# Kernel tuning notes

Hardware: AMD Instinct MI355X
Metric: run time of the kernel (lower is better)

Reference implementation:

```python
import jax, jax.numpy as jnp
import numpy as np

N_NODES = 50000
N_EDGES = 800000
HIDDEN = 128
N_GRAPHS = 32
EPS = 1e-5  # GraphNorm eps


def setup_inputs() -> dict:
    key = jax.random.key(0)
    ks = jax.random.split(key, 8)
    x = jax.random.normal(ks[0], (N_NODES, HIDDEN), dtype=jnp.float32)
    edge_index = jax.random.randint(ks[1], (2, N_EDGES), 0, N_NODES, dtype=jnp.int64)
    batch = jnp.sort(jax.random.randint(ks[2], (N_NODES,), 0, N_GRAPHS, dtype=jnp.int64))
    s = 1.0 / np.sqrt(HIDDEN)
    # SAGEConv: lin_l (applied to aggregated neighbors, with bias) and lin_r (root, no bias)
    W_l = jax.random.normal(ks[3], (HIDDEN, HIDDEN), dtype=jnp.float32) * s
    b_l = jnp.zeros((HIDDEN,), dtype=jnp.float32)
    W_r = jax.random.normal(ks[4], (HIDDEN, HIDDEN), dtype=jnp.float32) * s
    # GraphNorm params: weight, bias, mean_scale (alpha)
    gn_weight = jnp.ones((HIDDEN,), dtype=jnp.float32)
    gn_bias = jnp.zeros((HIDDEN,), dtype=jnp.float32)
    gn_mean_scale = jnp.ones((HIDDEN,), dtype=jnp.float32)
    return {
        "x": x, "edge_index": edge_index, "batch": batch,
        "W_l": W_l, "b_l": b_l, "W_r": W_r,
        "gn_weight": gn_weight, "gn_bias": gn_bias, "gn_mean_scale": gn_mean_scale,
    }


def reference(x, edge_index, batch, W_l, b_l, W_r, gn_weight, gn_bias, gn_mean_scale):
    src, dst = edge_index[0], edge_index[1]
    n = x.shape[0]
    # --- SAGEConv: mean aggregation of source features at destination ---
    msg_sum = jax.ops.segment_sum(x[src], dst, num_segments=n)          # [N, D]
    deg = jax.ops.segment_sum(jnp.ones((src.shape[0],), x.dtype), dst, num_segments=n)
    agg = msg_sum / jnp.maximum(deg, 1.0)[:, None]
    out = agg @ W_l + b_l + x @ W_r                                      # [N, D]
    # --- GraphNorm: per-graph mean/var with learnable mean scale alpha ---
    g_cnt = jax.ops.segment_sum(jnp.ones((n,), x.dtype), batch, num_segments=N_GRAPHS)[:, None]
    g_cnt = jnp.maximum(g_cnt, 1.0)
    mean = jax.ops.segment_sum(out, batch, num_segments=N_GRAPHS) / g_cnt  # [G, D]
    sub = out - gn_mean_scale * mean[batch]
    var = jax.ops.segment_sum(sub * sub, batch, num_segments=N_GRAPHS) / g_cnt
    normed = gn_weight * sub / jnp.sqrt(var[batch] + EPS) + gn_bias
    # --- exact GELU (torch nn.GELU default), dropout = identity (eval), residual ---
    return jax.nn.gelu(normed, approximate=False) + x
```

## Files before the change

### kernel.cpp

```cpp
#include <hip/hip_runtime.h>
#include <math.h>

#define NN 50000
#define NE 800000
#define HD 128
#define NG 32
#define GN_EPS 1e-5f
#define NSH 8

#define NBLK_R 250
#define CH_R   3200
#define NBUCK  196
#define NBB    (NBUCK * NBLK_R)
#define NCHS   ((NBB + 255) / 256)
#define DCAP   8192
#define PREP_BLKS 3125

typedef __bf16 v8bf __attribute__((ext_vector_type(8)));
typedef float f32x4 __attribute__((ext_vector_type(4)));

#define ROWPTR_OFF 0
#define BB_OFF     50016
#define CS_OFF     99016
#define GSUMS_OFF  99280
#define GSQS_OFF   132048
#define GCNTS_OFF  164816
#define MEAN_OFF   165072
#define RSTD_OFF   169168
#define SRCS_OFF   173264
#define PSRC_OFF   573264
#define PDLOW_OFF  973264
#define WPACK_OFF  1173264
#define ABUF_OFF   1189648
#define OBF_OFF    7589648
#define MEMSET_INTS (32768 + 32768 + 256)

__device__ __forceinline__ unsigned short f2bf(float f) {
  unsigned int u = __float_as_uint(f);
  u = (u + 0x7fffu + ((u >> 16) & 1u)) >> 16;
  return (unsigned short)u;
}
__device__ __forceinline__ float bf_lo(unsigned int u) { return __uint_as_float(u << 16); }
__device__ __forceinline__ float bf_hi(unsigned int u) { return __uint_as_float(u & 0xffff0000u); }

__global__ __launch_bounds__(256) void prep_rhist_k(const float* __restrict__ x,
    const float* __restrict__ Wl, const float* __restrict__ Wr,
    unsigned short* __restrict__ Abuf, unsigned short* __restrict__ wp,
    int* __restrict__ zbase, const int* __restrict__ ei, int* __restrict__ bb) {
  __shared__ int h[NBUCK];
  int tid = threadIdx.x;
  if (blockIdx.x < PREP_BLKS) {
    int i = blockIdx.x * 256 + tid;
    if (i < MEMSET_INTS) zbase[i] = 0;
    if (i < 32768) {
      int e = i & 7, lane = (i >> 3) & 63, nt = (i >> 9) & 7, ks = i >> 12;
      int k = ks * 32 + (lane >> 4) * 8 + e;
      int c = nt * 16 + (lane & 15);
      float v = (k < HD) ? Wl[k * HD + c] : Wr[(k - HD) * HD + c];
      wp[i] = f2bf(v);
    }
    if (i < NN * 16) {
      int n = i >> 4, seg = i & 15;
      const float* src = x + (size_t)n * HD + seg * 8;
      float4 v0 = *(const float4*)(src);
      float4 v1 = *(const float4*)(src + 4);
      uint4 o;
      o.x = (unsigned)f2bf(v0.x) | ((unsigned)f2bf(v0.y) << 16);
      o.y = (unsigned)f2bf(v0.z) | ((unsigned)f2bf(v0.w) << 16);
      o.z = (unsigned)f2bf(v1.x) | ((unsigned)f2bf(v1.y) << 16);
      o.w = (unsigned)f2bf(v1.z) | ((unsigned)f2bf(v1.w) << 16);
      *(uint4*)(Abuf + (size_t)n * 256 + 128 + seg * 8) = o;
    }
  } else {
    int b = blockIdx.x - PREP_BLKS;
    for (int i = tid; i < NBUCK; i += 256) h[i] = 0;
    __syncthreads();
    int base = b * CH_R;
    for (int j = tid; j < CH_R / 4; j += 256) {
      int4 d = *(const int4*)(ei + NE + base + j * 4);
      atomicAdd(&h[d.x >> 8], 1);
      atomicAdd(&h[d.y >> 8], 1);
      atomicAdd(&h[d.z >> 8], 1);
      atomicAdd(&h[d.w >> 8], 1);
    }
    __syncthreads();
    for (int i = tid; i < NBUCK; i += 256) bb[i * NBLK_R + b] = h[i];
  }
}

__global__ __launch_bounds__(256) void csum_k(const int* __restrict__ bb,
                                              int* __restrict__ cs) {
  __shared__ int red[4];
  int i = blockIdx.x * 256 + threadIdx.x;
  int v = (i < NBB) ? bb[i] : 0;
#pragma unroll
  for (int off = 32; off; off >>= 1) v += __shfl_down(v, off, 64);
  if ((threadIdx.x & 63) == 0) red[threadIdx.x >> 6] = v;
  __syncthreads();
  if (threadIdx.x == 0) cs[blockIdx.x] = red[0] + red[1] + red[2] + red[3];
}

__global__ __launch_bounds__(256) void cfill_k(int* __restrict__ bb,
                                               const int* __restrict__ cs) {
  __shared__ int sb[256];
  __shared__ int s[256];
  int t = threadIdx.x;
  sb[t] = (t < NCHS) ? cs[t] : 0;
  int i = blockIdx.x * 256 + t;
  int c = (i < NBB) ? bb[i] : 0;
  s[t] = c;
  __syncthreads();
#pragma unroll
  for (int off = 1; off < 256; off <<= 1) {
    int u1 = (t >= off) ? sb[t - off] : 0;
    int u2 = (t >= off) ? s[t - off] : 0;
    __syncthreads();
    sb[t] += u1;
    s[t] += u2;
    __syncthreads();
  }
  int chunkpre = (blockIdx.x == 0) ? 0 : sb[blockIdx.x - 1];
  if (i < NBB) bb[i] = chunkpre + s[t] - c;
}

__global__ __launch_bounds__(256) void rscatter_k(const int* __restrict__ ei,
    const int* __restrict__ bb, unsigned short* __restrict__ psrc,
    unsigned char* __restrict__ pdlow) {
  __shared__ int cur[NBUCK];
  int tid = threadIdx.x, b = blockIdx.x;
  for (int i = tid; i < NBUCK; i += 256) cur[i] = bb[i * NBLK_R + b];
  __syncthreads();
  int base = b * CH_R;
  for (int j = tid; j < CH_R / 4; j += 256) {
    int4 s4 = *(const int4*)(ei + base + j * 4);
    int4 d4 = *(const int4*)(ei + NE + base + j * 4);
    int p;
    p = atomicAdd(&cur[d4.x >> 8], 1); psrc[p] = (unsigned short)s4.x; pdlow[p] = (unsigned char)(d4.x & 255);
    p = atomicAdd(&cur[d4.y >> 8], 1); psrc[p] = (unsigned short)s4.y; pdlow[p] = (unsigned char)(d4.y & 255);
    p = atomicAdd(&cur[d4.z >> 8], 1); psrc[p] = (unsigned short)s4.z; pdlow[p] = (unsigned char)(d4.z & 255);
    p = atomicAdd(&cur[d4.w >> 8], 1); psrc[p] = (unsigned short)s4.w; pdlow[p] = (unsigned char)(d4.w & 255);
  }
}

__global__ __launch_bounds__(256) void rfinal_k(const int* __restrict__ bb,
    const unsigned short* __restrict__ psrc, const unsigned char* __restrict__ pdlow,
    unsigned short* __restrict__ srcs, int* __restrict__ rowptr) {
  __shared__ unsigned short ssrc[DCAP];
  __shared__ unsigned short sout[DCAP];
  __shared__ unsigned char sdl[DCAP];
  __shared__ int h2[256], scn[256], cur2[256];
  int tid = threadIdx.x, k = blockIdx.x;
  int segB = bb[k * NBLK_R];
  int segE = (k == NBUCK - 1) ? NE : bb[(k + 1) * NBLK_R];
  int cnt = segE - segB;
  for (int j = tid; j < cnt; j += 256) {
    ssrc[j] = psrc[segB + j];
    sdl[j] = pdlow[segB + j];
  }
  h2[tid] = 0;
  __syncthreads();
  for (int j = tid; j < cnt; j += 256) atomicAdd(&h2[sdl[j]], 1);
  __syncthreads();
  scn[tid] = h2[tid];
  __syncthreads();
#pragma unroll
  for (int off = 1; off < 256; off <<= 1) {
    int u = (tid >= off) ? scn[tid - off] : 0;
    __syncthreads();
    scn[tid] += u;
    __syncthreads();
  }
  int excl = scn[tid] - h2[tid];
  cur2[tid] = excl;
  int dst = k * 256 + tid;
  if (dst < NN) rowptr[dst] = segB + excl;
  if (dst == NN - 1) rowptr[NN] = NE;
  __syncthreads();
  for (int j = tid; j < cnt; j += 256) {
    int p = atomicAdd(&cur2[sdl[j]], 1);
    sout[p] = ssrc[j];
  }
  __syncthreads();
  for (int j = tid; j < cnt; j += 256) srcs[segB + j] = sout[j];
}

__global__ __launch_bounds__(256) void gather_k(const int* __restrict__ rowptr,
    const unsigned short* __restrict__ srcs, unsigned short* Abuf) {
  int t = blockIdx.x * 256 + threadIdx.x;
  int n = t >> 4, q = t & 15;
  if (n >= NN) return;
  int b = rowptr[n], e = rowptr[n + 1];
  float a0=0,a1=0,a2=0,a3=0,a4=0,a5=0,a6=0,a7=0;
  int i = b;
  for (; i + 1 < e; i += 2) {
    int s0 = srcs[i], s1 = srcs[i + 1];
    uint4 v0 = *(const uint4*)(Abuf + (size_t)s0 * 256 + 128 + q * 8);
    uint4 v1 = *(const uint4*)(Abuf + (size_t)s1 * 256 + 128 + q * 8);
    a0 += bf_lo(v0.x) + bf_lo(v1.x);  a1 += bf_hi(v0.x) + bf_hi(v1.x);
    a2 += bf_lo(v0.y) + bf_lo(v1.y);  a3 += bf_hi(v0.y) + bf_hi(v1.y);
    a4 += bf_lo(v0.z) + bf_lo(v1.z);  a5 += bf_hi(v0.z) + bf_hi(v1.z);
    a6 += bf_lo(v0.w) + bf_lo(v1.w);  a7 += bf_hi(v0.w) + bf_hi(v1.w);
  }
  if (i < e) {
    int s0 = srcs[i];
    uint4 v0 = *(const uint4*)(Abuf + (size_t)s0 * 256 + 128 + q * 8);
    a0 += bf_lo(v0.x); a1 += bf_hi(v0.x);
    a2 += bf_lo(v0.y); a3 += bf_hi(v0.y);
    a4 += bf_lo(v0.z); a5 += bf_hi(v0.z);
    a6 += bf_lo(v0.w); a7 += bf_hi(v0.w);
  }
  float inv = 1.0f / fmaxf((float)(e - b), 1.0f);
  uint4 o;
  o.x = (unsigned)f2bf(a0 * inv) | ((unsigned)f2bf(a1 * inv) << 16);
  o.y = (unsigned)f2bf(a2 * inv) | ((unsigned)f2bf(a3 * inv) << 16);
  o.z = (unsigned)f2bf(a4 * inv) | ((unsigned)f2bf(a5 * inv) << 16);
  o.w = (unsigned)f2bf(a6 * inv) | ((unsigned)f2bf(a7 * inv) << 16);
  *(uint4*)(Abuf + (size_t)n * 256 + q * 8) = o;
}

__global__ __launch_bounds__(256) void gemm_k(const unsigned short* __restrict__ Abuf,
    const unsigned short* __restrict__ wp, const float* __restrict__ bl,
    const int* __restrict__ batch, unsigned short* __restrict__ obf,
    float* __restrict__ gsumS, float* __restrict__ gsqS,
    float* __restrict__ gcntS) {
  __shared__ float lsum[16][136];
  __shared__ float lsq[16][136];
  __shared__ unsigned char ridx[64];
  __shared__ int sg0, snrun;
  int tid = threadIdx.x;
  int base0 = blockIdx.x * 64;
  int nvalid = min(64, NN - base0);
  if (tid == 0) {
    int g0 = batch[base0];
    sg0 = g0;
    snrun = batch[base0 + nvalid - 1] - g0 + 1;
  }
  __syncthreads();
  if (tid < 64)
    ridx[tid] = (tid < nvalid) ? (unsigned char)(batch[base0 + tid] - sg0)
                               : (unsigned char)0;
  __syncthreads();

  int shard = blockIdx.x & 7;
  float* gs = gsumS + shard * (NG * HD);
  float* gq = gsqS + shard * (NG * HD);
  float* gc = gcntS + shard * NG;

  int wave = tid >> 6;
  int lane = tid & 63;
  int base = base0 + wave * 16;
  int row = lane & 15, kg = lane >> 4;
  int node = base + row;
  if (node > NN - 1) node = NN - 1;
  const unsigned short* arow = Abuf + (size_t)node * 256 + kg * 8;
  f32x4 acc[8] = {};
#pragma unroll
  for (int ks = 0; ks < 8; ++ks) {
    v8bf a = __builtin_bit_cast(v8bf, *(const uint4*)(arow + ks * 32));
    const unsigned short* wrow = wp + ks * 4096 + lane * 8;
#pragma unroll
    for (int nt = 0; nt < 8; ++nt) {
      v8bf b = __builtin_bit_cast(v8bf, *(const uint4*)(wrow + nt * 512));
      acc[nt] = __builtin_amdgcn_mfma_f32_16x16x32_bf16(a, b, acc[nt], 0, 0, 0);
    }
  }
  int c0 = lane & 15;
  float bv[8];
#pragma unroll
  for (int nt = 0; nt < 8; ++nt) bv[nt] = bl[nt * 16 + c0];

  if (snrun == 1) {
    float ps0[8] = {}, pq0[8] = {};
#pragma unroll
    for (int j = 0; j < 4; ++j) {
      int n = base0 + wave * 16 + kg * 4 + j;
      if (n >= NN) break;
      unsigned short* orow = obf + (size_t)n * HD;
#pragma unroll
      for (int nt = 0; nt < 8; ++nt) {
        float v = acc[nt][j] + bv[nt];
        orow[nt * 16 + c0] = f2bf(v);
        ps0[nt] += v;
        pq0[nt] += v * v;
      }
    }
    int r = wave * 4 + kg;
#pragma unroll
    for (int nt = 0; nt < 8; ++nt) {
      lsum[r][nt * 16 + c0] = ps0[nt];
      lsq[r][nt * 16 + c0] = pq0[nt];
    }
    __syncthreads();
    if (tid < HD) {
      float s = 0.0f, q = 0.0f;
#pragma unroll
      for (int r2 = 0; r2 < 16; ++r2) { s += lsum[r2][tid]; q += lsq[r2][tid]; }
      atomicAdd(gs + sg0 * HD + tid, s);
      atomicAdd(gq + sg0 * HD + tid, q);
    }
    if (tid == 0) atomicAdd(gc + sg0, (float)nvalid);
  } else if (snrun == 2) {
    float ps0[8] = {}, pq0[8] = {}, ps1[8] = {}, pq1[8] = {};
#pragma unroll
    for (int j = 0; j < 4; ++j) {
      int rb = wave * 16 + kg * 4 + j;
      int n = base0 + rb;
      if (n >= NN) break;
      unsigned short* orow = obf + (size_t)n * HD;
      bool b1 = (ridx[rb] != 0);
#pragma unroll
      for (int nt = 0; nt < 8; ++nt) {
        float v = acc[nt][j] + bv[nt];
        orow[nt * 16 + c0] = f2bf(v);
        if (b1) { ps1[nt] += v; pq1[nt] += v * v; }
        else    { ps0[nt] += v; pq0[nt] += v * v; }
      }
    }
    int r = wave * 4 + kg;
#pragma unroll
    for (int nt = 0; nt < 8; ++nt) {
      lsum[r][nt * 16 + c0] = ps0[nt];
      lsq[r][nt * 16 + c0] = pq0[nt];
    }
    __syncthreads();
    if (tid < HD) {
      float s = 0.0f, q = 0.0f;
#pragma unroll
      for (int r2 = 0; r2 < 16; ++r2) { s += lsum[r2][tid]; q += lsq[r2][tid]; }
      atomicAdd(gs + sg0 * HD + tid, s);
      atomicAdd(gq + sg0 * HD + tid, q);
    }
    __syncthreads();
#pragma unroll
    for (int nt = 0; nt < 8; ++nt) {
      lsum[r][nt * 16 + c0] = ps1[nt];
      lsq[r][nt * 16 + c0] = pq1[nt];
    }
    __syncthreads();
    if (tid < HD) {
      float s = 0.0f, q = 0.0f;
#pragma unroll
      for (int r2 = 0; r2 < 16; ++r2) { s += lsum[r2][tid]; q += lsq[r2][tid]; }
      atomicAdd(gs + (sg0 + 1) * HD + tid, s);
      atomicAdd(gq + (sg0 + 1) * HD + tid, q);
    }
    if (tid == 0) {
      int n0 = 0;
      for (int r2 = 0; r2 < nvalid; ++r2) n0 += (ridx[r2] == 0);
      atomicAdd(gc + sg0, (float)n0);
      atomicAdd(gc + sg0 + 1, (float)(nvalid - n0));
    }
  } else {
#pragma unroll
    for (int j = 0; j < 4; ++j) {
      int rb = wave * 16 + kg * 4 + j;
      int n = base0 + rb;
      if (n >= NN) break;
      unsigned short* orow = obf + (size_t)n * HD;
      int g = sg0 + ridx[rb];
#pragma unroll
      for (int nt = 0; nt < 8; ++nt) {
        float v = acc[nt][j] + bv[nt];
        orow[nt * 16 + c0] = f2bf(v);
        atomicAdd(gs + g * HD + nt * 16 + c0, v);
        atomicAdd(gq + g * HD + nt * 16 + c0, v * v);
      }
    }
    if (tid < nvalid) atomicAdd(gc + batch[base0 + tid], 1.0f);
  }
}

__global__ __launch_bounds__(256) void finalize_k(const float* __restrict__ gsumS,
    const float* __restrict__ gsqS, const float* __restrict__ gcntS,
    const float* __restrict__ alpha, float* __restrict__ mean,
    float* __restrict__ rstd) {
  int i = blockIdx.x * 256 + threadIdx.x;
  if (i >= NG * HD) return;
  int g = i >> 7, d = i & 127;
  float s = 0.0f, q = 0.0f, cnt = 0.0f;
#pragma unroll
  for (int sh = 0; sh < NSH; ++sh) {
    s += gsumS[sh * (NG * HD) + i];
    q += gsqS[sh * (NG * HD) + i];
    cnt += gcntS[sh * NG + g];
  }
  cnt = fmaxf(cnt, 1.0f);
  float mu = s / cnt;
  float a = alpha[d];
  float var = q / cnt - mu * mu * (2.0f * a - a * a);
  mean[i] = mu;
  rstd[i] = rsqrtf(fmaxf(var, 0.0f) + GN_EPS);
}

__global__ __launch_bounds__(256) void final_k(const unsigned short* __restrict__ obf,
    float* __restrict__ out, const float* __restrict__ x,
    const int* __restrict__ batch, const float* __restrict__ mean,
    const float* __restrict__ rstd, const float* __restrict__ alpha,
    const float* __restrict__ gw, const float* __restrict__ gb) {
  size_t i = ((size_t)blockIdx.x * 256 + threadIdx.x) * 4;
  if (i >= (size_t)NN * HD) return;
  int n = (int)(i >> 7);
  int d = (int)(i & 127);
  int g = batch[n];
  uint2 ov = *(const uint2*)(obf + i);
  float4 xv = *(const float4*)(x + i);
  float4 al = *(const float4*)(alpha + d);
  float4 w  = *(const float4*)(gw + d);
  float4 b  = *(const float4*)(gb + d);
  float4 mn = *(const float4*)(mean + (size_t)g * HD + d);
  float4 rs = *(const float4*)(rstd + (size_t)g * HD + d);
  float vv[4] = {bf_lo(ov.x), bf_hi(ov.x), bf_lo(ov.y), bf_hi(ov.y)};
  float xx[4] = {xv.x, xv.y, xv.z, xv.w};
  float aa[4] = {al.x, al.y, al.z, al.w};
  float ww[4] = {w.x, w.y, w.z, w.w};
  float bb2[4] = {b.x, b.y, b.z, b.w};
  float mm[4] = {mn.x, mn.y, mn.z, mn.w};
  float rr[4] = {rs.x, rs.y, rs.z, rs.w};
  float r[4];
#pragma unroll
  for (int c = 0; c < 4; ++c) {
    float sub = vv[c] - aa[c] * mm[c];
    float nm  = ww[c] * sub * rr[c] + bb2[c];
    float ge  = 0.5f * nm * (1.0f + erff(nm * 0.70710678118654752f));
    r[c] = ge + xx[c];
  }
  float4 res = {r[0], r[1], r[2], r[3]};
  *(float4*)(out + i) = res;
}

extern "C" void kernel_launch(void* const* d_in, const int* in_sizes, int n_in,
                              void* d_out, int out_size, void* d_ws, size_t ws_size,
                              hipStream_t stream) {
  const float* x     = (const float*)d_in[0];
  const int*   ei    = (const int*)d_in[1];
  const int*   batch = (const int*)d_in[2];
  const float* Wl    = (const float*)d_in[3];
  const float* bl    = (const float*)d_in[4];
  const float* Wr    = (const float*)d_in[5];
  const float* gw    = (const float*)d_in[6];
  const float* gb    = (const float*)d_in[7];
  const float* alpha = (const float*)d_in[8];

  float* out = (float*)d_out;
  int*   wsi = (int*)d_ws;
  float* wsf = (float*)d_ws;
  int* rowptr = wsi + ROWPTR_OFF;
  int* bb     = wsi + BB_OFF;
  int* cs     = wsi + CS_OFF;
  float* gsumS = wsf + GSUMS_OFF;
  float* gsqS  = wsf + GSQS_OFF;
  float* gcntS = wsf + GCNTS_OFF;
  float* mean  = wsf + MEAN_OFF;
  float* rstd  = wsf + RSTD_OFF;
  unsigned short* srcs  = (unsigned short*)(wsi + SRCS_OFF);
  unsigned short* psrc  = (unsigned short*)(wsi + PSRC_OFF);
  unsigned char*  pdlow = (unsigned char*)(wsi + PDLOW_OFF);
  unsigned short* wpack = (unsigned short*)(wsi + WPACK_OFF);
  unsigned short* Abuf  = (unsigned short*)(wsi + ABUF_OFF);
  unsigned short* obf   = (unsigned short*)(wsi + OBF_OFF);

  prep_rhist_k<<<PREP_BLKS + NBLK_R, 256, 0, stream>>>(
      x, Wl, Wr, Abuf, wpack, (int*)(wsf + GSUMS_OFF), ei, bb);

  csum_k<<<NCHS, 256, 0, stream>>>(bb, cs);
  cfill_k<<<NCHS, 256, 0, stream>>>(bb, cs);
  rscatter_k<<<NBLK_R, 256, 0, stream>>>(ei, bb, psrc, pdlow);
  rfinal_k<<<NBUCK, 256, 0, stream>>>(bb, psrc, pdlow, srcs, rowptr);

  gather_k<<<(NN * 16 + 255) / 256, 256, 0, stream>>>(rowptr, srcs, Abuf);

  gemm_k<<<(NN + 63) / 64, 256, 0, stream>>>(Abuf, wpack, bl, batch, obf,
                                             gsumS, gsqS, gcntS);

  finalize_k<<<16, 256, 0, stream>>>(gsumS, gsqS, gcntS, alpha, mean, rstd);

  final_k<<<(NN * HD / 4 + 255) / 256, 256, 0, stream>>>(
      obf, out, x, batch, mean, rstd, alpha, gw, gb);
}
```

Before: 108.4 us.

## Partition neighbor gather by source range and enlarge radix sort block count

The gather kernel now makes four passes over each node's edge list and in each pass loads only source rows from one quarter of the node range. The aim is to keep concurrently accessed rows within a cache-sized window. The radix histogram and scatter stages use 800 blocks of 1000 edges instead of 250 of 3200, and the scan kernel moves to 1024-thread blocks to cover the larger bucket-by-block table. In exchange, the edge index list is read four times per node with a branch per edge, and the prefix scan has more entries to process.

```diff
diff --git a/kernel.cpp b/kernel.cpp
--- a/kernel.cpp
+++ b/kernel.cpp
@@ -8,31 +8,34 @@
 #define GN_EPS 1e-5f
 #define NSH 8
 
-#define NBLK_R 250
-#define CH_R   3200
+#define NBLK_R 800
+#define CH_R   1000
 #define NBUCK  196
 #define NBB    (NBUCK * NBLK_R)
 #define NCHS   ((NBB + 255) / 256)
 #define DCAP   8192
 #define PREP_BLKS 3125
 
+#define GP 4
+#define GW (NN / GP)
+
 typedef __bf16 v8bf __attribute__((ext_vector_type(8)));
 typedef float f32x4 __attribute__((ext_vector_type(4)));
 
 #define ROWPTR_OFF 0
 #define BB_OFF     50016
-#define CS_OFF     99016
-#define GSUMS_OFF  99280
-#define GSQS_OFF   132048
-#define GCNTS_OFF  164816
-#define MEAN_OFF   165072
-#define RSTD_OFF   169168
-#define SRCS_OFF   173264
-#define PSRC_OFF   573264
-#define PDLOW_OFF  973264
-#define WPACK_OFF  1173264
-#define ABUF_OFF   1189648
-#define OBF_OFF    7589648
+#define CS_OFF     206816
+#define GSUMS_OFF  207840
+#define GSQS_OFF   240608
+#define GCNTS_OFF  273376
+#define MEAN_OFF   273632
+#define RSTD_OFF   277728
+#define SRCS_OFF   281824
+#define PSRC_OFF   681824
+#define PDLOW_OFF  1081824
+#define WPACK_OFF  1281824
+#define ABUF_OFF   1298208
+#define OBF_OFF    7698208
 #define MEMSET_INTS (32768 + 32768 + 256)
 
 __device__ __forceinline__ unsigned short f2bf(float f) {
@@ -76,8 +79,8 @@
     for (int i = tid; i < NBUCK; i += 256) h[i] = 0;
     __syncthreads();
     int base = b * CH_R;
-    for (int j = tid; j < CH_R / 4; j += 256) {
-      int4 d = *(const int4*)(ei + NE + base + j * 4);
+    if (tid < CH_R / 4) {
+      int4 d = *(const int4*)(ei + NE + base + tid * 4);
       atomicAdd(&h[d.x >> 8], 1);
       atomicAdd(&h[d.y >> 8], 1);
       atomicAdd(&h[d.z >> 8], 1);
@@ -100,18 +103,17 @@
   if (threadIdx.x == 0) cs[blockIdx.x] = red[0] + red[1] + red[2] + red[3];
 }
 
-__global__ __launch_bounds__(256) void cfill_k(int* __restrict__ bb,
-                                               const int* __restrict__ cs) {
-  __shared__ int sb[256];
-  __shared__ int s[256];
+__global__ __launch_bounds__(1024) void cfill_k(int* __restrict__ bb,
+                                                const int* __restrict__ cs) {
+  __shared__ int sb[1024];
+  __shared__ int s[1024];
   int t = threadIdx.x;
   sb[t] = (t < NCHS) ? cs[t] : 0;
-  int i = blockIdx.x * 256 + t;
+  int i = blockIdx.x * 1024 + t;
   int c = (i < NBB) ? bb[i] : 0;
   s[t] = c;
   __syncthreads();
-#pragma unroll
-  for (int off = 1; off < 256; off <<= 1) {
+  for (int off = 1; off < 1024; off <<= 1) {
     int u1 = (t >= off) ? sb[t - off] : 0;
     int u2 = (t >= off) ? s[t - off] : 0;
     __syncthreads();
@@ -119,7 +121,7 @@
     s[t] += u2;
     __syncthreads();
   }
-  int chunkpre = (blockIdx.x == 0) ? 0 : sb[blockIdx.x - 1];
+  int chunkpre = (blockIdx.x == 0) ? 0 : sb[blockIdx.x * 4 - 1];
   if (i < NBB) bb[i] = chunkpre + s[t] - c;
 }
 
@@ -131,9 +133,9 @@
   for (int i = tid; i < NBUCK; i += 256) cur[i] = bb[i * NBLK_R + b];
   __syncthreads();
   int base = b * CH_R;
-  for (int j = tid; j < CH_R / 4; j += 256) {
-    int4 s4 = *(const int4*)(ei + base + j * 4);
-    int4 d4 = *(const int4*)(ei + NE + base + j * 4);
+  if (tid < CH_R / 4) {
+    int4 s4 = *(const int4*)(ei + base + tid * 4);
+    int4 d4 = *(const int4*)(ei + NE + base + tid * 4);
     int p;
     p = atomicAdd(&cur[d4.x >> 8], 1); psrc[p] = (unsigned short)s4.x; pdlow[p] = (unsigned char)(d4.x & 255);
     p = atomicAdd(&cur[d4.y >> 8], 1); psrc[p] = (unsigned short)s4.y; pdlow[p] = (unsigned char)(d4.y & 255);
@@ -191,23 +193,19 @@
   if (n >= NN) return;
   int b = rowptr[n], e = rowptr[n + 1];
   float a0=0,a1=0,a2=0,a3=0,a4=0,a5=0,a6=0,a7=0;
-  int i = b;
-  for (; i + 1 < e; i += 2) {
-    int s0 = srcs[i], s1 = srcs[i + 1];
-    uint4 v0 = *(const uint4*)(Abuf + (size_t)s0 * 256 + 128 + q * 8);
-    uint4 v1 = *(const uint4*)(Abuf + (size_t)s1 * 256 + 128 + q * 8);
-    a0 += bf_lo(v0.x) + bf_lo(v1.x);  a1 += bf_hi(v0.x) + bf_hi(v1.x);
-    a2 += bf_lo(v0.y) + bf_lo(v1.y);  a3 += bf_hi(v0.y) + bf_hi(v1.y);
-    a4 += bf_lo(v0.z) + bf_lo(v1.z);  a5 += bf_hi(v0.z) + bf_hi(v1.z);
-    a6 += bf_lo(v0.w) + bf_lo(v1.w);  a7 += bf_hi(v0.w) + bf_hi(v1.w);
-  }
-  if (i < e) {
-    int s0 = srcs[i];
-    uint4 v0 = *(const uint4*)(Abuf + (size_t)s0 * 256 + 128 + q * 8);
-    a0 += bf_lo(v0.x); a1 += bf_hi(v0.x);
-    a2 += bf_lo(v0.y); a3 += bf_hi(v0.y);
-    a4 += bf_lo(v0.z); a5 += bf_hi(v0.z);
-    a6 += bf_lo(v0.w); a7 += bf_hi(v0.w);
+#pragma unroll 1
+  for (int p = 0; p < GP; ++p) {
+    int lo = p * GW, hi = lo + GW;
+    for (int i = b; i < e; ++i) {
+      int s0 = srcs[i];
+      if (s0 >= lo && s0 < hi) {
+        uint4 v0 = *(const uint4*)(Abuf + (size_t)s0 * 256 + 128 + q * 8);
+        a0 += bf_lo(v0.x); a1 += bf_hi(v0.x);
+        a2 += bf_lo(v0.y); a3 += bf_hi(v0.y);
+        a4 += bf_lo(v0.z); a5 += bf_hi(v0.z);
+        a6 += bf_lo(v0.w); a7 += bf_hi(v0.w);
+      }
+    }
   }
   float inv = 1.0f / fmaxf((float)(e - b), 1.0f);
   uint4 o;
@@ -463,7 +461,7 @@
       x, Wl, Wr, Abuf, wpack, (int*)(wsf + GSUMS_OFF), ei, bb);
 
   csum_k<<<NCHS, 256, 0, stream>>>(bb, cs);
-  cfill_k<<<NCHS, 256, 0, stream>>>(bb, cs);
+  cfill_k<<<(NBB + 1023) / 1024, 1024, 0, stream>>>(bb, cs);
   rscatter_k<<<NBLK_R, 256, 0, stream>>>(ei, bb, psrc, pdlow);
   rfinal_k<<<NBUCK, 256, 0, stream>>>(bb, psrc, pdlow, srcs, rowptr);
 
```

After: 169.5 us. 1.56x slower.
